# Kernel tuning notes

Measured on AMD Instinct MI355X. Metric: run time of the kernel, lower is better.

Reference implementation:

```python
import jax, jax.numpy as jnp
from jax import lax
import numpy as np

B, T, C, D = 16384, 64, 2, 4  # batch, timesteps(nodes), coords, gat out dim
NEG_SLOPE = 0.2

def setup_inputs() -> dict:
    key = jax.random.key(0)
    ks = jax.random.split(key, 9)
    s = lambda *sh: 0.1
    return {
        "x":      jax.random.normal(ks[0], (B, T, C), jnp.float32),
        "W_gat":  jax.random.normal(ks[1], (D, C), jnp.float32) * 0.5,
        "a_attn": jax.random.normal(ks[2], (1, 2 * D), jnp.float32) * 0.5,
        "conv_w": jax.random.normal(ks[3], (T, T, 3), jnp.float32) * 0.05,
        "conv_b": jax.random.normal(ks[4], (T,), jnp.float32) * 0.05,
        "dec_w1": jax.random.normal(ks[5], (T * 8, T * 2), jnp.float32) * 0.05,
        "dec_b1": jax.random.normal(ks[6], (T * 8,), jnp.float32) * 0.05,
        "dec_w2": jax.random.normal(ks[7], (T * 2, T * 8), jnp.float32) * 0.05,
        "dec_b2": jax.random.normal(ks[8], (T * 2,), jnp.float32) * 0.05,
    }

def reference(x, W_gat, a_attn, conv_w, conv_b, dec_w1, dec_b1, dec_w2, dec_b2):
    b, t, c = x.shape
    # --- GAT layer on fully connected graph (no self loops), batched over B ---
    z = jnp.einsum('btc,dc->btd', x, W_gat)            # [B,T,D]
    a_src, a_dst = a_attn[0, :D], a_attn[0, D:]
    es = z @ a_src                                      # [B,T] contribution of edge source i
    ed = z @ a_dst                                      # [B,T] contribution of edge dest j
    e = jax.nn.leaky_relu(es[:, :, None] + ed[:, None, :], NEG_SLOPE)  # e[b,i,j], edge i->j
    no_self = ~jnp.eye(t, dtype=bool)
    e = jnp.where(no_self[None], e, -jnp.inf)           # graph has no self-loops
    alpha = jax.nn.softmax(e, axis=1)                   # softmax over incoming sources i per dst j
    h = jnp.einsum('bij,bid->bjd', alpha, z)            # [B,T,D] aggregated node features
    # --- conv1d: channels = timesteps, length = D, kernel 3 -> length D-2 ---
    out_conv = lax.conv_general_dilated(h, conv_w, (1,), 'VALID',
                                        dimension_numbers=('NCH', 'OIH', 'NCH'))
    out_conv = out_conv + conv_b[None, :, None]         # [B,T,D-2] == [B,T,2]
    # --- MLP decoder on flattened conv output ---
    flat = out_conv.reshape(b, t * 2)
    hdec = jax.nn.relu(flat @ dec_w1.T + dec_b1)
    dec = hdec @ dec_w2.T + dec_b2
    encoder_out = out_conv[:, None]                     # stacked unsqueeze(0): [B,1,T,2]
    decoded = dec.reshape(b, t, c)                      # [B,T,2]
    return encoder_out, decoded
```

## Files before the change

kernel.cpp:

```cpp
#include <hip/hip_runtime.h>


typedef __attribute__((ext_vector_type(8))) short bf16x8;
typedef __attribute__((ext_vector_type(4))) float f32x4;
typedef _Float16 h2 __attribute__((ext_vector_type(2)));

__device__ __forceinline__ unsigned short f2bf(float f) {
    unsigned int u = __builtin_bit_cast(unsigned int, f);
    return (unsigned short)((u + 0x7FFFu + ((u >> 16) & 1u)) >> 16);
}
__device__ __forceinline__ unsigned int pack2bf(float a, float b) {
    return (unsigned int)f2bf(a) | ((unsigned int)f2bf(b) << 16);
}

#define SWZ(row) (((row) & 7) << 3)

__global__ void k0_prep(const float* __restrict__ w1, const float* __restrict__ w2,
                        const float* __restrict__ cw, const float* __restrict__ cb,
                        unsigned short* __restrict__ w1c, unsigned short* __restrict__ w2c,
                        unsigned short* __restrict__ wcvc, float* __restrict__ biasf) {
    const int i = blockIdx.x * 256 + threadIdx.x;
    const int rem = i & 511, ln = rem >> 3, e = rem & 7;
    const int r = ln & 15, g = ln >> 4;
    {
        const int frag = i >> 9, nb = frag >> 2, kb = frag & 3;
        w1c[i] = f2bf(w1[(nb * 16 + r) * 128 + kb * 32 + g * 8 + e]);
    }
    {
        const int frag = i >> 9, mb = frag >> 4, np = frag & 15;
        w2c[i] = f2bf(w2[(mb * 16 + r) * 512 + np * 32 + g * 8 + e]);
    }
    if (i < 32768) {
        const int frag = i >> 9, fb = frag >> 3, kc = frag & 7;
        const int f = fb * 16 + r, kd = kc * 32 + g * 8 + e;
        const int o = f >> 1, s = f & 1, node = kd >> 2, d = kd & 3;
        const int k = d - s;
        const float v = (k >= 0 && k < 3) ? cw[o * 192 + node * 3 + k] : 0.f;
        wcvc[i] = f2bf(v);
    }
    if (i < 128) biasf[i] = cb[i >> 1];
}

__global__ __launch_bounds__(256, 4) void k_fused(
    const float* __restrict__ x,
    const float* __restrict__ W_gat,
    const float* __restrict__ a_attn,
    const unsigned short* __restrict__ w1c,
    const unsigned short* __restrict__ w2c,
    const unsigned short* __restrict__ wcvc,
    const float* __restrict__ biasf,
    const float* __restrict__ b1,
    const float* __restrict__ b2,
    float* __restrict__ enc_out,
    float* __restrict__ dec_out)
{
    __shared__ __align__(16) unsigned char smem[28672];
    unsigned short* h_lds    = (unsigned short*)smem;
    unsigned short* flat_lds = (unsigned short*)(smem + 8192);
    unsigned short* scr16    = (unsigned short*)(smem + 12288);
    unsigned short* hdec_lds = (unsigned short*)(smem + 12288);

    const int tid = threadIdx.x, lane = tid & 63, wv = tid >> 6;
    const int r = lane & 15, g = lane >> 4;
    const int base = blockIdx.x * 16;
    const int l8 = lane * 8;

    {
        const float Wg00 = W_gat[0], Wg01 = W_gat[1], Wg10 = W_gat[2], Wg11 = W_gat[3];
        const float Wg20 = W_gat[4], Wg21 = W_gat[5], Wg30 = W_gat[6], Wg31 = W_gat[7];
        const float as0 = a_attn[0], as1 = a_attn[1], as2 = a_attn[2], as3 = a_attn[3];
        const float ad0 = a_attn[4], ad1 = a_attn[5], ad2 = a_attn[6], ad3 = a_attn[7];
        const float cs0 = as0 * Wg00 + as1 * Wg10 + as2 * Wg20 + as3 * Wg30;
        const float cs1 = as0 * Wg01 + as1 * Wg11 + as2 * Wg21 + as3 * Wg31;
        const float cd0 = ad0 * Wg00 + ad1 * Wg10 + ad2 * Wg20 + ad3 * Wg30;
        const float cd1 = ad0 * Wg01 + ad1 * Wg11 + ad2 * Wg21 + ad3 * Wg31;
        const float L2E = 1.4426950408889634f;
        const float SL = 0.2f;

        h2 uvh[4], UVh[4], xyh[4];
        float xf0[4], xf1[4];

        #pragma unroll
        for (int t = 0; t < 4; ++t) {
            const float2 xv = ((const float2*)x)[(size_t)(base + wv * 4 + t) * 64 + lane];
            const float es = xv.x * cs0 + xv.y * cs1;
            const float ed = xv.x * cd0 + xv.y * cd1;
            float M = es;
            #pragma unroll
            for (int m = 32; m; m >>= 1) M = fmaxf(M, __shfl_xor(M, m));
            const float um = (es - M) * L2E;
            const _Float16 uh = (_Float16)__builtin_amdgcn_exp2f(um);
            const _Float16 vh = (_Float16)__builtin_amdgcn_exp2f(SL * um);
            const float tt = M + ed;
            const float mj = fmaxf(tt, SL * tt);
            const _Float16 Uh = (_Float16)__builtin_amdgcn_exp2f((ed + M - mj) * L2E);
            const _Float16 Vh = (_Float16)__builtin_amdgcn_exp2f((SL * (ed + M) - mj) * L2E);
            const _Float16 x0h = (_Float16)xv.x, x1h = (_Float16)xv.y;

            unsigned short* rowp = scr16 + (wv * 4 + t) * 256;
            rowp[lane]       = __builtin_bit_cast(unsigned short, uh);
            rowp[64 + lane]  = __builtin_bit_cast(unsigned short, vh);
            rowp[128 + lane] = __builtin_bit_cast(unsigned short, x0h);
            rowp[192 + lane] = __builtin_bit_cast(unsigned short, x1h);

            uvh[t] = (h2){uh, vh};
            UVh[t] = (h2){Uh, Vh};
            xyh[t] = (h2){x0h, x1h};
            xf0[t] = (float)x0h; xf1[t] = (float)x1h;
        }

        const h2 one2 = {(_Float16)1.0f, (_Float16)1.0f};

        #pragma unroll
        for (int t = 0; t < 4; ++t) {
            const uint4* up = (const uint4*)(scr16 + (wv * 4 + t) * 256);
            const h2 UU = (h2){UVh[t].x, UVh[t].x};
            const h2 VV = (h2){UVh[t].y, UVh[t].y};
            float S = 0.f, A0 = 0.f, A1 = 0.f;
            #pragma unroll 4
            for (int k = 0; k < 8; ++k) {
                const uint4 uq  = up[k];
                const uint4 vq  = up[8 + k];
                const uint4 x0q = up[16 + k];
                const uint4 x1q = up[24 + k];
                const unsigned* ua  = (const unsigned*)&uq;
                const unsigned* va  = (const unsigned*)&vq;
                const unsigned* x0a = (const unsigned*)&x0q;
                const unsigned* x1a = (const unsigned*)&x1q;
                #pragma unroll
                for (int p = 0; p < 4; ++p) {
                    const h2 u2  = __builtin_bit_cast(h2, ua[p]);
                    const h2 v2  = __builtin_bit_cast(h2, va[p]);
                    const h2 P2  = __builtin_elementwise_max(u2 * UU, v2 * VV);
#if __has_builtin(__builtin_amdgcn_fdot2)
                    S  = __builtin_amdgcn_fdot2(P2, one2, S, false);
                    A0 = __builtin_amdgcn_fdot2(P2, __builtin_bit_cast(h2, x0a[p]), A0, false);
                    A1 = __builtin_amdgcn_fdot2(P2, __builtin_bit_cast(h2, x1a[p]), A1, false);
#else
                    const h2 xa = __builtin_bit_cast(h2, x0a[p]);
                    const h2 xb = __builtin_bit_cast(h2, x1a[p]);
                    S  += (float)P2.x + (float)P2.y;
                    A0 += (float)P2.x * (float)xa.x + (float)P2.y * (float)xa.y;
                    A1 += (float)P2.x * (float)xb.x + (float)P2.y * (float)xb.y;
#endif
                }
            }
            const h2 pm = uvh[t] * UVh[t];
            const _Float16 pSh = (pm.x > pm.y) ? pm.x : pm.y;
            const float pS = (float)pSh;
            S -= pS;
            A0 -= pS * xf0[t];
            A1 -= pS * xf1[t];
            const float rs = 1.0f / S;
            const float h0 = (Wg00 * A0 + Wg01 * A1) * rs;
            const float h1 = (Wg10 * A0 + Wg11 * A1) * rs;
            const float h2v = (Wg20 * A0 + Wg21 * A1) * rs;
            const float h3 = (Wg30 * A0 + Wg31 * A1) * rs;
            const int lr = wv * 4 + t;
            const int hidx = (lr * 256 + lane * 4) ^ SWZ(lr);
            *(uint2*)(&h_lds[hidx]) = make_uint2(pack2bf(h0, h1), pack2bf(h2v, h3));
        }
    }
    __syncthreads();

    f32x4 accc[2];
    accc[0] = (f32x4){0.f, 0.f, 0.f, 0.f};
    accc[1] = (f32x4){0.f, 0.f, 0.f, 0.f};
    #pragma unroll
    for (int kc = 0; kc < 8; ++kc) {
        const bf16x8 hf  = *(const bf16x8*)(&h_lds[(r * 256 + kc * 32 + g * 8) ^ SWZ(r)]);
        const bf16x8 wfa = *(const bf16x8*)(wcvc + ((wv * 8 + kc) << 9) + l8);
        const bf16x8 wfb = *(const bf16x8*)(wcvc + (((wv + 4) * 8 + kc) << 9) + l8);
        accc[0] = __builtin_amdgcn_mfma_f32_16x16x32_bf16(wfa, hf, accc[0], 0, 0, 0);
        accc[1] = __builtin_amdgcn_mfma_f32_16x16x32_bf16(wfb, hf, accc[1], 0, 0, 0);
    }
    #pragma unroll
    for (int q = 0; q < 2; ++q) {
        const int f0 = (wv + q * 4) * 16 + g * 4;
        const float4 bs = *(const float4*)(biasf + f0);
        const float v0 = accc[q][0] + bs.x, v1 = accc[q][1] + bs.y;
        const float v2 = accc[q][2] + bs.z, v3 = accc[q][3] + bs.w;
        *(float4*)(enc_out + (size_t)(base + r) * 128 + f0) = make_float4(v0, v1, v2, v3);
        const int fidx = (r * 128 + f0) ^ SWZ(r);
        *(uint2*)(&flat_lds[fidx]) = make_uint2(pack2bf(v0, v1), pack2bf(v2, v3));
    }
    __syncthreads();

    bf16x8 ff1[4];
    #pragma unroll
    for (int kb = 0; kb < 4; ++kb)
        ff1[kb] = *(const bf16x8*)(&flat_lds[(r * 128 + kb * 32 + g * 8) ^ SWZ(r)]);
    #pragma unroll
    for (int t = 0; t < 8; ++t) {
        const int nb = wv * 8 + t;
        f32x4 a1 = (f32x4){0.f, 0.f, 0.f, 0.f};
        #pragma unroll
        for (int kb = 0; kb < 4; ++kb) {
            const bf16x8 wf = *(const bf16x8*)(w1c + (((nb << 2) + kb) << 9) + l8);
            a1 = __builtin_amdgcn_mfma_f32_16x16x32_bf16(wf, ff1[kb], a1, 0, 0, 0);
        }
        const int n0 = nb * 16 + g * 4;
        const float4 bs = *(const float4*)(b1 + n0);
        const float v0 = fmaxf(a1[0] + bs.x, 0.f);
        const float v1 = fmaxf(a1[1] + bs.y, 0.f);
        const float v2 = fmaxf(a1[2] + bs.z, 0.f);
        const float v3 = fmaxf(a1[3] + bs.w, 0.f);
        const int hdidx = (r * 512 + n0) ^ SWZ(r);
        *(uint2*)(&hdec_lds[hdidx]) = make_uint2(pack2bf(v0, v1), pack2bf(v2, v3));
    }
    __syncthreads();

    f32x4 acc2[2];
    acc2[0] = (f32x4){0.f, 0.f, 0.f, 0.f};
    acc2[1] = (f32x4){0.f, 0.f, 0.f, 0.f};
    #pragma unroll
    for (int np = 0; np < 16; ++np) {
        const bf16x8 hfd = *(const bf16x8*)(&hdec_lds[(r * 512 + np * 32 + g * 8) ^ SWZ(r)]);
        const bf16x8 wfa = *(const bf16x8*)(w2c + (((wv * 16) + np) << 9) + l8);
        const bf16x8 wfb = *(const bf16x8*)(w2c + ((((wv + 4) * 16) + np) << 9) + l8);
        acc2[0] = __builtin_amdgcn_mfma_f32_16x16x32_bf16(wfa, hfd, acc2[0], 0, 0, 0);
        acc2[1] = __builtin_amdgcn_mfma_f32_16x16x32_bf16(wfb, hfd, acc2[1], 0, 0, 0);
    }
    #pragma unroll
    for (int q = 0; q < 2; ++q) {
        const int m0 = (wv + q * 4) * 16 + g * 4;
        const float4 bs = *(const float4*)(b2 + m0);
        *(float4*)(dec_out + (size_t)(base + r) * 128 + m0) =
            make_float4(acc2[q][0] + bs.x, acc2[q][1] + bs.y,
                        acc2[q][2] + bs.z, acc2[q][3] + bs.w);
    }
}

extern "C" void kernel_launch(void* const* d_in, const int* in_sizes, int n_in,
                              void* d_out, int out_size, void* d_ws, size_t ws_size,
                              hipStream_t stream) {
    const float* x      = (const float*)d_in[0];
    const float* W_gat  = (const float*)d_in[1];
    const float* a_attn = (const float*)d_in[2];
    const float* conv_w = (const float*)d_in[3];
    const float* conv_b = (const float*)d_in[4];
    const float* dec_w1 = (const float*)d_in[5];
    const float* dec_b1 = (const float*)d_in[6];
    const float* dec_w2 = (const float*)d_in[7];
    const float* dec_b2 = (const float*)d_in[8];
    float* out = (float*)d_out;

    const int B = in_sizes[0] / 128;
    unsigned short* w1c  = (unsigned short*)d_ws;
    unsigned short* w2c  = w1c + 128 * 512;
    unsigned short* wcvc = w2c + 128 * 512;
    float* biasf = (float*)(wcvc + 64 * 512);

    k0_prep<<<256, 256, 0, stream>>>(dec_w1, dec_w2, conv_w, conv_b, w1c, w2c, wcvc, biasf);

    k_fused<<<B / 16, 256, 0, stream>>>(x, W_gat, a_attn, w1c, w2c, wcvc, biasf,
                                        dec_b1, dec_b2, out, out + (size_t)B * 128);
}
```

Measured before the change: 31.01 us.

## Process 32 batch rows per block to reuse weight fragments across two MFMA tiles

Each block now handles 32 batch elements instead of 16, so every weight fragment loaded from global memory (conv, dec_w1, dec_w2) feeds two MFMA tiles. The GAT phase is merged into a single per-row loop that prefetches the next x row while computing the current one. Shared memory doubles and launch bounds drop to 2 blocks per CU, which cuts weight-load traffic but halves the block count and may reduce occupancy and latency hiding.

```diff
diff --git a/kernel.cpp b/kernel.cpp
--- a/kernel.cpp
+++ b/kernel.cpp
@@ -41,7 +41,7 @@
     if (i < 128) biasf[i] = cb[i >> 1];
 }
 
-__global__ __launch_bounds__(256, 4) void k_fused(
+__global__ __launch_bounds__(256, 2) void k_fused(
     const float* __restrict__ x,
     const float* __restrict__ W_gat,
     const float* __restrict__ a_attn,
@@ -54,15 +54,15 @@
     float* __restrict__ enc_out,
     float* __restrict__ dec_out)
 {
-    __shared__ __align__(16) unsigned char smem[28672];
+    __shared__ __align__(16) unsigned char smem[57344];
     unsigned short* h_lds    = (unsigned short*)smem;
-    unsigned short* flat_lds = (unsigned short*)(smem + 8192);
-    unsigned short* scr16    = (unsigned short*)(smem + 12288);
-    unsigned short* hdec_lds = (unsigned short*)(smem + 12288);
+    unsigned short* flat_lds = (unsigned short*)(smem + 16384);
+    unsigned short* scr16    = (unsigned short*)(smem + 24576);
+    unsigned short* hdec_lds = (unsigned short*)(smem + 24576);
 
     const int tid = threadIdx.x, lane = tid & 63, wv = tid >> 6;
     const int r = lane & 15, g = lane >> 4;
-    const int base = blockIdx.x * 16;
+    const int base = blockIdx.x * 32;
     const int l8 = lane * 8;
 
     {
@@ -76,13 +76,15 @@
         const float cd1 = ad0 * Wg01 + ad1 * Wg11 + ad2 * Wg21 + ad3 * Wg31;
         const float L2E = 1.4426950408889634f;
         const float SL = 0.2f;
-
-        h2 uvh[4], UVh[4], xyh[4];
-        float xf0[4], xf1[4];
-
-        #pragma unroll
-        for (int t = 0; t < 4; ++t) {
-            const float2 xv = ((const float2*)x)[(size_t)(base + wv * 4 + t) * 64 + lane];
+        const h2 one2 = {(_Float16)1.0f, (_Float16)1.0f};
+
+        float2 xv = ((const float2*)x)[(size_t)(base + wv * 8) * 64 + lane];
+        #pragma unroll
+        for (int t = 0; t < 8; ++t) {
+            float2 xv_n;
+            if (t < 7) xv_n = ((const float2*)x)[(size_t)(base + wv * 8 + t + 1) * 64 + lane];
+            const int lr = wv * 8 + t;
+
             const float es = xv.x * cs0 + xv.y * cs1;
             const float ed = xv.x * cd0 + xv.y * cd1;
             float M = es;
@@ -97,25 +99,15 @@
             const _Float16 Vh = (_Float16)__builtin_amdgcn_exp2f((SL * (ed + M) - mj) * L2E);
             const _Float16 x0h = (_Float16)xv.x, x1h = (_Float16)xv.y;
 
-            unsigned short* rowp = scr16 + (wv * 4 + t) * 256;
+            unsigned short* rowp = scr16 + lr * 256;
             rowp[lane]       = __builtin_bit_cast(unsigned short, uh);
             rowp[64 + lane]  = __builtin_bit_cast(unsigned short, vh);
             rowp[128 + lane] = __builtin_bit_cast(unsigned short, x0h);
             rowp[192 + lane] = __builtin_bit_cast(unsigned short, x1h);
 
-            uvh[t] = (h2){uh, vh};
-            UVh[t] = (h2){Uh, Vh};
-            xyh[t] = (h2){x0h, x1h};
-            xf0[t] = (float)x0h; xf1[t] = (float)x1h;
-        }
-
-        const h2 one2 = {(_Float16)1.0f, (_Float16)1.0f};
-
-        #pragma unroll
-        for (int t = 0; t < 4; ++t) {
-            const uint4* up = (const uint4*)(scr16 + (wv * 4 + t) * 256);
-            const h2 UU = (h2){UVh[t].x, UVh[t].x};
-            const h2 VV = (h2){UVh[t].y, UVh[t].y};
+            const h2 UU = (h2){Uh, Uh};
+            const h2 VV = (h2){Vh, Vh};
+            const uint4* up = (const uint4*)rowp;
             float S = 0.f, A0 = 0.f, A1 = 0.f;
             #pragma unroll 4
             for (int k = 0; k < 8; ++k) {
@@ -129,9 +121,9 @@
                 const unsigned* x1a = (const unsigned*)&x1q;
                 #pragma unroll
                 for (int p = 0; p < 4; ++p) {
-                    const h2 u2  = __builtin_bit_cast(h2, ua[p]);
-                    const h2 v2  = __builtin_bit_cast(h2, va[p]);
-                    const h2 P2  = __builtin_elementwise_max(u2 * UU, v2 * VV);
+                    const h2 u2 = __builtin_bit_cast(h2, ua[p]);
+                    const h2 v2 = __builtin_bit_cast(h2, va[p]);
+                    const h2 P2 = __builtin_elementwise_max(u2 * UU, v2 * VV);
 #if __has_builtin(__builtin_amdgcn_fdot2)
                     S  = __builtin_amdgcn_fdot2(P2, one2, S, false);
                     A0 = __builtin_amdgcn_fdot2(P2, __builtin_bit_cast(h2, x0a[p]), A0, false);
@@ -145,89 +137,115 @@
 #endif
                 }
             }
-            const h2 pm = uvh[t] * UVh[t];
+            const h2 pm = (h2){uh, vh} * (h2){Uh, Vh};
             const _Float16 pSh = (pm.x > pm.y) ? pm.x : pm.y;
             const float pS = (float)pSh;
             S -= pS;
-            A0 -= pS * xf0[t];
-            A1 -= pS * xf1[t];
+            A0 -= pS * (float)x0h;
+            A1 -= pS * (float)x1h;
             const float rs = 1.0f / S;
             const float h0 = (Wg00 * A0 + Wg01 * A1) * rs;
             const float h1 = (Wg10 * A0 + Wg11 * A1) * rs;
             const float h2v = (Wg20 * A0 + Wg21 * A1) * rs;
             const float h3 = (Wg30 * A0 + Wg31 * A1) * rs;
-            const int lr = wv * 4 + t;
             const int hidx = (lr * 256 + lane * 4) ^ SWZ(lr);
             *(uint2*)(&h_lds[hidx]) = make_uint2(pack2bf(h0, h1), pack2bf(h2v, h3));
+            xv = xv_n;
         }
     }
     __syncthreads();
 
-    f32x4 accc[2];
-    accc[0] = (f32x4){0.f, 0.f, 0.f, 0.f};
-    accc[1] = (f32x4){0.f, 0.f, 0.f, 0.f};
+    f32x4 accc[2][2];
+    #pragma unroll
+    for (int q = 0; q < 2; ++q)
+        #pragma unroll
+        for (int tl = 0; tl < 2; ++tl) accc[q][tl] = (f32x4){0.f, 0.f, 0.f, 0.f};
     #pragma unroll
     for (int kc = 0; kc < 8; ++kc) {
-        const bf16x8 hf  = *(const bf16x8*)(&h_lds[(r * 256 + kc * 32 + g * 8) ^ SWZ(r)]);
         const bf16x8 wfa = *(const bf16x8*)(wcvc + ((wv * 8 + kc) << 9) + l8);
         const bf16x8 wfb = *(const bf16x8*)(wcvc + (((wv + 4) * 8 + kc) << 9) + l8);
-        accc[0] = __builtin_amdgcn_mfma_f32_16x16x32_bf16(wfa, hf, accc[0], 0, 0, 0);
-        accc[1] = __builtin_amdgcn_mfma_f32_16x16x32_bf16(wfb, hf, accc[1], 0, 0, 0);
+        #pragma unroll
+        for (int tl = 0; tl < 2; ++tl) {
+            const int row = tl * 16 + r;
+            const bf16x8 hf = *(const bf16x8*)(&h_lds[(row * 256 + kc * 32 + g * 8) ^ SWZ(r)]);
+            accc[0][tl] = __builtin_amdgcn_mfma_f32_16x16x32_bf16(wfa, hf, accc[0][tl], 0, 0, 0);
+            accc[1][tl] = __builtin_amdgcn_mfma_f32_16x16x32_bf16(wfb, hf, accc[1][tl], 0, 0, 0);
+        }
     }
     #pragma unroll
     for (int q = 0; q < 2; ++q) {
         const int f0 = (wv + q * 4) * 16 + g * 4;
         const float4 bs = *(const float4*)(biasf + f0);
-        const float v0 = accc[q][0] + bs.x, v1 = accc[q][1] + bs.y;
-        const float v2 = accc[q][2] + bs.z, v3 = accc[q][3] + bs.w;
-        *(float4*)(enc_out + (size_t)(base + r) * 128 + f0) = make_float4(v0, v1, v2, v3);
-        const int fidx = (r * 128 + f0) ^ SWZ(r);
-        *(uint2*)(&flat_lds[fidx]) = make_uint2(pack2bf(v0, v1), pack2bf(v2, v3));
+        #pragma unroll
+        for (int tl = 0; tl < 2; ++tl) {
+            const int row = tl * 16 + r;
+            const float v0 = accc[q][tl][0] + bs.x, v1 = accc[q][tl][1] + bs.y;
+            const float v2 = accc[q][tl][2] + bs.z, v3 = accc[q][tl][3] + bs.w;
+            *(float4*)(enc_out + (size_t)(base + row) * 128 + f0) = make_float4(v0, v1, v2, v3);
+            const int fidx = (row * 128 + f0) ^ SWZ(r);
+            *(uint2*)(&flat_lds[fidx]) = make_uint2(pack2bf(v0, v1), pack2bf(v2, v3));
+        }
     }
     __syncthreads();
 
-    bf16x8 ff1[4];
-    #pragma unroll
-    for (int kb = 0; kb < 4; ++kb)
-        ff1[kb] = *(const bf16x8*)(&flat_lds[(r * 128 + kb * 32 + g * 8) ^ SWZ(r)]);
+    bf16x8 ff1[2][4];
+    #pragma unroll
+    for (int tl = 0; tl < 2; ++tl)
+        #pragma unroll
+        for (int kb = 0; kb < 4; ++kb)
+            ff1[tl][kb] = *(const bf16x8*)(&flat_lds[((tl * 16 + r) * 128 + kb * 32 + g * 8) ^ SWZ(r)]);
     #pragma unroll
     for (int t = 0; t < 8; ++t) {
         const int nb = wv * 8 + t;
-        f32x4 a1 = (f32x4){0.f, 0.f, 0.f, 0.f};
+        f32x4 a1[2];
+        a1[0] = (f32x4){0.f, 0.f, 0.f, 0.f};
+        a1[1] = (f32x4){0.f, 0.f, 0.f, 0.f};
         #pragma unroll
         for (int kb = 0; kb < 4; ++kb) {
             const bf16x8 wf = *(const bf16x8*)(w1c + (((nb << 2) + kb) << 9) + l8);
-            a1 = __builtin_amdgcn_mfma_f32_16x16x32_bf16(wf, ff1[kb], a1, 0, 0, 0);
+            a1[0] = __builtin_amdgcn_mfma_f32_16x16x32_bf16(wf, ff1[0][kb], a1[0], 0, 0, 0);
+            a1[1] = __builtin_amdgcn_mfma_f32_16x16x32_bf16(wf, ff1[1][kb], a1[1], 0, 0, 0);
         }
         const int n0 = nb * 16 + g * 4;
         const float4 bs = *(const float4*)(b1 + n0);
-        const float v0 = fmaxf(a1[0] + bs.x, 0.f);
-        const float v1 = fmaxf(a1[1] + bs.y, 0.f);
-        const float v2 = fmaxf(a1[2] + bs.z, 0.f);
-        const float v3 = fmaxf(a1[3] + bs.w, 0.f);
-        const int hdidx = (r * 512 + n0) ^ SWZ(r);
-        *(uint2*)(&hdec_lds[hdidx]) = make_uint2(pack2bf(v0, v1), pack2bf(v2, v3));
+        #pragma unroll
+        for (int tl = 0; tl < 2; ++tl) {
+            const float v0 = fmaxf(a1[tl][0] + bs.x, 0.f);
+            const float v1 = fmaxf(a1[tl][1] + bs.y, 0.f);
+            const float v2 = fmaxf(a1[tl][2] + bs.z, 0.f);
+            const float v3 = fmaxf(a1[tl][3] + bs.w, 0.f);
+            const int hdidx = ((tl * 16 + r) * 512 + n0) ^ SWZ(r);
+            *(uint2*)(&hdec_lds[hdidx]) = make_uint2(pack2bf(v0, v1), pack2bf(v2, v3));
+        }
     }
     __syncthreads();
 
-    f32x4 acc2[2];
-    acc2[0] = (f32x4){0.f, 0.f, 0.f, 0.f};
-    acc2[1] = (f32x4){0.f, 0.f, 0.f, 0.f};
+    f32x4 acc2[2][2];
+    #pragma unroll
+    for (int q = 0; q < 2; ++q)
+        #pragma unroll
+        for (int tl = 0; tl < 2; ++tl) acc2[q][tl] = (f32x4){0.f, 0.f, 0.f, 0.f};
     #pragma unroll
     for (int np = 0; np < 16; ++np) {
-        const bf16x8 hfd = *(const bf16x8*)(&hdec_lds[(r * 512 + np * 32 + g * 8) ^ SWZ(r)]);
         const bf16x8 wfa = *(const bf16x8*)(w2c + (((wv * 16) + np) << 9) + l8);
         const bf16x8 wfb = *(const bf16x8*)(w2c + ((((wv + 4) * 16) + np) << 9) + l8);
-        acc2[0] = __builtin_amdgcn_mfma_f32_16x16x32_bf16(wfa, hfd, acc2[0], 0, 0, 0);
-        acc2[1] = __builtin_amdgcn_mfma_f32_16x16x32_bf16(wfb, hfd, acc2[1], 0, 0, 0);
+        #pragma unroll
+        for (int tl = 0; tl < 2; ++tl) {
+            const bf16x8 hfd = *(const bf16x8*)(&hdec_lds[((tl * 16 + r) * 512 + np * 32 + g * 8) ^ SWZ(r)]);
+            acc2[0][tl] = __builtin_amdgcn_mfma_f32_16x16x32_bf16(wfa, hfd, acc2[0][tl], 0, 0, 0);
+            acc2[1][tl] = __builtin_amdgcn_mfma_f32_16x16x32_bf16(wfb, hfd, acc2[1][tl], 0, 0, 0);
+        }
     }
     #pragma unroll
     for (int q = 0; q < 2; ++q) {
         const int m0 = (wv + q * 4) * 16 + g * 4;
         const float4 bs = *(const float4*)(b2 + m0);
-        *(float4*)(dec_out + (size_t)(base + r) * 128 + m0) =
-            make_float4(acc2[q][0] + bs.x, acc2[q][1] + bs.y,
-                        acc2[q][2] + bs.z, acc2[q][3] + bs.w);
+        #pragma unroll
+        for (int tl = 0; tl < 2; ++tl) {
+            *(float4*)(dec_out + (size_t)(base + tl * 16 + r) * 128 + m0) =
+                make_float4(acc2[q][tl][0] + bs.x, acc2[q][tl][1] + bs.y,
+                            acc2[q][tl][2] + bs.z, acc2[q][tl][3] + bs.w);
+        }
     }
 }
 
@@ -253,6 +271,6 @@
 
     k0_prep<<<256, 256, 0, stream>>>(dec_w1, dec_w2, conv_w, conv_b, w1c, w2c, wcvc, biasf);
 
-    k_fused<<<B / 16, 256, 0, stream>>>(x, W_gat, a_attn, w1c, w2c, wcvc, biasf,
+    k_fused<<<B / 32, 256, 0, stream>>>(x, W_gat, a_attn, w1c, w2c, wcvc, biasf,
                                         dec_b1, dec_b2, out, out + (size_t)B * 128);
 }
```

Measured after the change: 32.16 us. 3.7% more time.

## Split fused kernel work across eight waves per block instead of four

Applied to the files above, without the earlier changes.

Launches 512 threads per block so each wave handles two batch rows in the GAT stage and half as many output tiles in the conv and decoder MFMA stages. The per-wave MFMA chains are split into two independent accumulators over K halves to shorten dependency chains, and the next x row is prefetched before the current one is processed. The aim is more waves in flight and less serial work per wave to hide latency. In exchange, the larger block with launch bounds (512,3) changes the register budget and occupancy, and the block-wide syncs now cover more waves.

```diff
diff --git a/kernel.cpp b/kernel.cpp
--- a/kernel.cpp
+++ b/kernel.cpp
@@ -41,7 +41,7 @@
     if (i < 128) biasf[i] = cb[i >> 1];
 }
 
-__global__ __launch_bounds__(256, 4) void k_fused(
+__global__ __launch_bounds__(512, 3) void k_fused(
     const float* __restrict__ x,
     const float* __restrict__ W_gat,
     const float* __restrict__ a_attn,
@@ -76,13 +76,15 @@
         const float cd1 = ad0 * Wg01 + ad1 * Wg11 + ad2 * Wg21 + ad3 * Wg31;
         const float L2E = 1.4426950408889634f;
         const float SL = 0.2f;
-
-        h2 uvh[4], UVh[4], xyh[4];
-        float xf0[4], xf1[4];
-
+        const h2 one2 = {(_Float16)1.0f, (_Float16)1.0f};
+
+        float2 xv = ((const float2*)x)[(size_t)(base + wv * 2) * 64 + lane];
         #pragma unroll
-        for (int t = 0; t < 4; ++t) {
-            const float2 xv = ((const float2*)x)[(size_t)(base + wv * 4 + t) * 64 + lane];
+        for (int t = 0; t < 2; ++t) {
+            float2 xv_n;
+            if (t == 0) xv_n = ((const float2*)x)[(size_t)(base + wv * 2 + 1) * 64 + lane];
+            const int lr = wv * 2 + t;
+
             const float es = xv.x * cs0 + xv.y * cs1;
             const float ed = xv.x * cd0 + xv.y * cd1;
             float M = es;
@@ -97,25 +99,15 @@
             const _Float16 Vh = (_Float16)__builtin_amdgcn_exp2f((SL * (ed + M) - mj) * L2E);
             const _Float16 x0h = (_Float16)xv.x, x1h = (_Float16)xv.y;
 
-            unsigned short* rowp = scr16 + (wv * 4 + t) * 256;
+            unsigned short* rowp = scr16 + lr * 256;
             rowp[lane]       = __builtin_bit_cast(unsigned short, uh);
             rowp[64 + lane]  = __builtin_bit_cast(unsigned short, vh);
             rowp[128 + lane] = __builtin_bit_cast(unsigned short, x0h);
             rowp[192 + lane] = __builtin_bit_cast(unsigned short, x1h);
 
-            uvh[t] = (h2){uh, vh};
-            UVh[t] = (h2){Uh, Vh};
-            xyh[t] = (h2){x0h, x1h};
-            xf0[t] = (float)x0h; xf1[t] = (float)x1h;
-        }
-
-        const h2 one2 = {(_Float16)1.0f, (_Float16)1.0f};
-
-        #pragma unroll
-        for (int t = 0; t < 4; ++t) {
-            const uint4* up = (const uint4*)(scr16 + (wv * 4 + t) * 256);
-            const h2 UU = (h2){UVh[t].x, UVh[t].x};
-            const h2 VV = (h2){UVh[t].y, UVh[t].y};
+            const h2 UU = (h2){Uh, Uh};
+            const h2 VV = (h2){Vh, Vh};
+            const uint4* up = (const uint4*)rowp;
             float S = 0.f, A0 = 0.f, A1 = 0.f;
             #pragma unroll 4
             for (int k = 0; k < 8; ++k) {
@@ -129,9 +121,9 @@
                 const unsigned* x1a = (const unsigned*)&x1q;
                 #pragma unroll
                 for (int p = 0; p < 4; ++p) {
-                    const h2 u2  = __builtin_bit_cast(h2, ua[p]);
-                    const h2 v2  = __builtin_bit_cast(h2, va[p]);
-                    const h2 P2  = __builtin_elementwise_max(u2 * UU, v2 * VV);
+                    const h2 u2 = __builtin_bit_cast(h2, ua[p]);
+                    const h2 v2 = __builtin_bit_cast(h2, va[p]);
+                    const h2 P2 = __builtin_elementwise_max(u2 * UU, v2 * VV);
 #if __has_builtin(__builtin_amdgcn_fdot2)
                     S  = __builtin_amdgcn_fdot2(P2, one2, S, false);
                     A0 = __builtin_amdgcn_fdot2(P2, __builtin_bit_cast(h2, x0a[p]), A0, false);
@@ -145,41 +137,41 @@
 #endif
                 }
             }
-            const h2 pm = uvh[t] * UVh[t];
+            const h2 pm = (h2){uh, vh} * (h2){Uh, Vh};
             const _Float16 pSh = (pm.x > pm.y) ? pm.x : pm.y;
             const float pS = (float)pSh;
             S -= pS;
-            A0 -= pS * xf0[t];
-            A1 -= pS * xf1[t];
+            A0 -= pS * (float)x0h;
+            A1 -= pS * (float)x1h;
             const float rs = 1.0f / S;
             const float h0 = (Wg00 * A0 + Wg01 * A1) * rs;
             const float h1 = (Wg10 * A0 + Wg11 * A1) * rs;
             const float h2v = (Wg20 * A0 + Wg21 * A1) * rs;
             const float h3 = (Wg30 * A0 + Wg31 * A1) * rs;
-            const int lr = wv * 4 + t;
             const int hidx = (lr * 256 + lane * 4) ^ SWZ(lr);
             *(uint2*)(&h_lds[hidx]) = make_uint2(pack2bf(h0, h1), pack2bf(h2v, h3));
+            xv = xv_n;
         }
     }
     __syncthreads();
 
-    f32x4 accc[2];
-    accc[0] = (f32x4){0.f, 0.f, 0.f, 0.f};
-    accc[1] = (f32x4){0.f, 0.f, 0.f, 0.f};
-    #pragma unroll
-    for (int kc = 0; kc < 8; ++kc) {
-        const bf16x8 hf  = *(const bf16x8*)(&h_lds[(r * 256 + kc * 32 + g * 8) ^ SWZ(r)]);
-        const bf16x8 wfa = *(const bf16x8*)(wcvc + ((wv * 8 + kc) << 9) + l8);
-        const bf16x8 wfb = *(const bf16x8*)(wcvc + (((wv + 4) * 8 + kc) << 9) + l8);
-        accc[0] = __builtin_amdgcn_mfma_f32_16x16x32_bf16(wfa, hf, accc[0], 0, 0, 0);
-        accc[1] = __builtin_amdgcn_mfma_f32_16x16x32_bf16(wfb, hf, accc[1], 0, 0, 0);
-    }
-    #pragma unroll
-    for (int q = 0; q < 2; ++q) {
-        const int f0 = (wv + q * 4) * 16 + g * 4;
+    f32x4 ca = (f32x4){0.f, 0.f, 0.f, 0.f};
+    f32x4 cb2 = (f32x4){0.f, 0.f, 0.f, 0.f};
+    #pragma unroll
+    for (int kc = 0; kc < 4; ++kc) {
+        const bf16x8 hf0 = *(const bf16x8*)(&h_lds[(r * 256 + kc * 32 + g * 8) ^ SWZ(r)]);
+        const bf16x8 hf1 = *(const bf16x8*)(&h_lds[(r * 256 + (kc + 4) * 32 + g * 8) ^ SWZ(r)]);
+        const bf16x8 wf0 = *(const bf16x8*)(wcvc + ((wv * 8 + kc) << 9) + l8);
+        const bf16x8 wf1 = *(const bf16x8*)(wcvc + ((wv * 8 + kc + 4) << 9) + l8);
+        ca  = __builtin_amdgcn_mfma_f32_16x16x32_bf16(wf0, hf0, ca, 0, 0, 0);
+        cb2 = __builtin_amdgcn_mfma_f32_16x16x32_bf16(wf1, hf1, cb2, 0, 0, 0);
+    }
+    {
+        const f32x4 cc = ca + cb2;
+        const int f0 = wv * 16 + g * 4;
         const float4 bs = *(const float4*)(biasf + f0);
-        const float v0 = accc[q][0] + bs.x, v1 = accc[q][1] + bs.y;
-        const float v2 = accc[q][2] + bs.z, v3 = accc[q][3] + bs.w;
+        const float v0 = cc[0] + bs.x, v1 = cc[1] + bs.y;
+        const float v2 = cc[2] + bs.z, v3 = cc[3] + bs.w;
         *(float4*)(enc_out + (size_t)(base + r) * 128 + f0) = make_float4(v0, v1, v2, v3);
         const int fidx = (r * 128 + f0) ^ SWZ(r);
         *(uint2*)(&flat_lds[fidx]) = make_uint2(pack2bf(v0, v1), pack2bf(v2, v3));
@@ -191,8 +183,8 @@
     for (int kb = 0; kb < 4; ++kb)
         ff1[kb] = *(const bf16x8*)(&flat_lds[(r * 128 + kb * 32 + g * 8) ^ SWZ(r)]);
     #pragma unroll
-    for (int t = 0; t < 8; ++t) {
-        const int nb = wv * 8 + t;
+    for (int t = 0; t < 4; ++t) {
+        const int nb = wv * 4 + t;
         f32x4 a1 = (f32x4){0.f, 0.f, 0.f, 0.f};
         #pragma unroll
         for (int kb = 0; kb < 4; ++kb) {
@@ -210,24 +202,23 @@
     }
     __syncthreads();
 
-    f32x4 acc2[2];
-    acc2[0] = (f32x4){0.f, 0.f, 0.f, 0.f};
-    acc2[1] = (f32x4){0.f, 0.f, 0.f, 0.f};
-    #pragma unroll
-    for (int np = 0; np < 16; ++np) {
-        const bf16x8 hfd = *(const bf16x8*)(&hdec_lds[(r * 512 + np * 32 + g * 8) ^ SWZ(r)]);
-        const bf16x8 wfa = *(const bf16x8*)(w2c + (((wv * 16) + np) << 9) + l8);
-        const bf16x8 wfb = *(const bf16x8*)(w2c + ((((wv + 4) * 16) + np) << 9) + l8);
-        acc2[0] = __builtin_amdgcn_mfma_f32_16x16x32_bf16(wfa, hfd, acc2[0], 0, 0, 0);
-        acc2[1] = __builtin_amdgcn_mfma_f32_16x16x32_bf16(wfb, hfd, acc2[1], 0, 0, 0);
-    }
-    #pragma unroll
-    for (int q = 0; q < 2; ++q) {
-        const int m0 = (wv + q * 4) * 16 + g * 4;
+    f32x4 d2a = (f32x4){0.f, 0.f, 0.f, 0.f};
+    f32x4 d2b = (f32x4){0.f, 0.f, 0.f, 0.f};
+    #pragma unroll
+    for (int np = 0; np < 8; ++np) {
+        const bf16x8 h0 = *(const bf16x8*)(&hdec_lds[(r * 512 + np * 32 + g * 8) ^ SWZ(r)]);
+        const bf16x8 h1 = *(const bf16x8*)(&hdec_lds[(r * 512 + (np + 8) * 32 + g * 8) ^ SWZ(r)]);
+        const bf16x8 w0 = *(const bf16x8*)(w2c + (((wv * 16) + np) << 9) + l8);
+        const bf16x8 w1 = *(const bf16x8*)(w2c + (((wv * 16) + np + 8) << 9) + l8);
+        d2a = __builtin_amdgcn_mfma_f32_16x16x32_bf16(w0, h0, d2a, 0, 0, 0);
+        d2b = __builtin_amdgcn_mfma_f32_16x16x32_bf16(w1, h1, d2b, 0, 0, 0);
+    }
+    {
+        const f32x4 dd = d2a + d2b;
+        const int m0 = wv * 16 + g * 4;
         const float4 bs = *(const float4*)(b2 + m0);
         *(float4*)(dec_out + (size_t)(base + r) * 128 + m0) =
-            make_float4(acc2[q][0] + bs.x, acc2[q][1] + bs.y,
-                        acc2[q][2] + bs.z, acc2[q][3] + bs.w);
+            make_float4(dd[0] + bs.x, dd[1] + bs.y, dd[2] + bs.z, dd[3] + bs.w);
     }
 }
 
@@ -253,6 +244,6 @@
 
     k0_prep<<<256, 256, 0, stream>>>(dec_w1, dec_w2, conv_w, conv_b, w1c, w2c, wcvc, biasf);
 
-    k_fused<<<B / 16, 256, 0, stream>>>(x, W_gat, a_attn, w1c, w2c, wcvc, biasf,
+    k_fused<<<B / 16, 512, 0, stream>>>(x, W_gat, a_attn, w1c, w2c, wcvc, biasf,
                                         dec_b1, dec_b2, out, out + (size_t)B * 128);
 }
```

New measurement: 32.53 us. 1.05x slower.

## Split fused kernel into attention and conv/decoder kernels via global staging

Applied to the files above, without the earlier changes.

The fused kernel is split in two. The first computes the GAT attention and writes bf16 h values in MFMA fragment order into the decoded output region as scratch. The second reads h directly from global memory for the conv MFMAs and then runs the decoder. The aim is lower register and LDS pressure per kernel and a software-prefetched x load. The cost is an extra launch plus a global round trip for h, and the scratch buffer relies on being overwritten in place, since the second kernel reads h from the same region it writes decoded results into.

```diff
diff --git a/kernel.cpp b/kernel.cpp
--- a/kernel.cpp
+++ b/kernel.cpp
@@ -41,10 +41,110 @@
     if (i < 128) biasf[i] = cb[i >> 1];
 }
 
-__global__ __launch_bounds__(256, 4) void k_fused(
+__global__ __launch_bounds__(256, 4) void k_attn(
     const float* __restrict__ x,
     const float* __restrict__ W_gat,
     const float* __restrict__ a_attn,
+    unsigned int* __restrict__ h_frag)
+{
+    __shared__ unsigned short scr16[16 * 256];
+
+    const int tid = threadIdx.x, lane = tid & 63, wv = tid >> 6;
+    const int base = blockIdx.x * 16;
+
+    const float Wg00 = W_gat[0], Wg01 = W_gat[1], Wg10 = W_gat[2], Wg11 = W_gat[3];
+    const float Wg20 = W_gat[4], Wg21 = W_gat[5], Wg30 = W_gat[6], Wg31 = W_gat[7];
+    const float as0 = a_attn[0], as1 = a_attn[1], as2 = a_attn[2], as3 = a_attn[3];
+    const float ad0 = a_attn[4], ad1 = a_attn[5], ad2 = a_attn[6], ad3 = a_attn[7];
+    const float cs0 = as0 * Wg00 + as1 * Wg10 + as2 * Wg20 + as3 * Wg30;
+    const float cs1 = as0 * Wg01 + as1 * Wg11 + as2 * Wg21 + as3 * Wg31;
+    const float cd0 = ad0 * Wg00 + ad1 * Wg10 + ad2 * Wg20 + ad3 * Wg30;
+    const float cd1 = ad0 * Wg01 + ad1 * Wg11 + ad2 * Wg21 + ad3 * Wg31;
+    const float L2E = 1.4426950408889634f;
+    const float SL = 0.2f;
+    const h2 one2 = {(_Float16)1.0f, (_Float16)1.0f};
+
+    const int j = lane;
+    unsigned int* outp = h_frag + (size_t)blockIdx.x * 2048
+                       + (j >> 3) * 256 + ((j >> 1) & 3) * 64 + (j & 1) * 2;
+
+    float2 xv = ((const float2*)x)[(size_t)(base + wv * 4) * 64 + lane];
+    #pragma unroll
+    for (int t = 0; t < 4; ++t) {
+        float2 xv_n;
+        if (t < 3) xv_n = ((const float2*)x)[(size_t)(base + wv * 4 + t + 1) * 64 + lane];
+        const int lr = wv * 4 + t;
+
+        const float es = xv.x * cs0 + xv.y * cs1;
+        const float ed = xv.x * cd0 + xv.y * cd1;
+        float M = es;
+        #pragma unroll
+        for (int m = 32; m; m >>= 1) M = fmaxf(M, __shfl_xor(M, m));
+        const float um = (es - M) * L2E;
+        const _Float16 uh = (_Float16)__builtin_amdgcn_exp2f(um);
+        const _Float16 vh = (_Float16)__builtin_amdgcn_exp2f(SL * um);
+        const float tt = M + ed;
+        const float mj = fmaxf(tt, SL * tt);
+        const _Float16 Uh = (_Float16)__builtin_amdgcn_exp2f((ed + M - mj) * L2E);
+        const _Float16 Vh = (_Float16)__builtin_amdgcn_exp2f((SL * (ed + M) - mj) * L2E);
+        const _Float16 x0h = (_Float16)xv.x, x1h = (_Float16)xv.y;
+
+        unsigned short* rowp = scr16 + lr * 256;
+        rowp[lane]       = __builtin_bit_cast(unsigned short, uh);
+        rowp[64 + lane]  = __builtin_bit_cast(unsigned short, vh);
+        rowp[128 + lane] = __builtin_bit_cast(unsigned short, x0h);
+        rowp[192 + lane] = __builtin_bit_cast(unsigned short, x1h);
+
+        const h2 UU = (h2){Uh, Uh};
+        const h2 VV = (h2){Vh, Vh};
+        const uint4* up = (const uint4*)rowp;
+        float S = 0.f, A0 = 0.f, A1 = 0.f;
+        #pragma unroll 4
+        for (int k = 0; k < 8; ++k) {
+            const uint4 uq  = up[k];
+            const uint4 vq  = up[8 + k];
+            const uint4 x0q = up[16 + k];
+            const uint4 x1q = up[24 + k];
+            const unsigned* ua  = (const unsigned*)&uq;
+            const unsigned* va  = (const unsigned*)&vq;
+            const unsigned* x0a = (const unsigned*)&x0q;
+            const unsigned* x1a = (const unsigned*)&x1q;
+            #pragma unroll
+            for (int p = 0; p < 4; ++p) {
+                const h2 u2 = __builtin_bit_cast(h2, ua[p]);
+                const h2 v2 = __builtin_bit_cast(h2, va[p]);
+                const h2 P2 = __builtin_elementwise_max(u2 * UU, v2 * VV);
+#if __has_builtin(__builtin_amdgcn_fdot2)
+                S  = __builtin_amdgcn_fdot2(P2, one2, S, false);
+                A0 = __builtin_amdgcn_fdot2(P2, __builtin_bit_cast(h2, x0a[p]), A0, false);
+                A1 = __builtin_amdgcn_fdot2(P2, __builtin_bit_cast(h2, x1a[p]), A1, false);
+#else
+                const h2 xa = __builtin_bit_cast(h2, x0a[p]);
+                const h2 xb = __builtin_bit_cast(h2, x1a[p]);
+                S  += (float)P2.x + (float)P2.y;
+                A0 += (float)P2.x * (float)xa.x + (float)P2.y * (float)xa.y;
+                A1 += (float)P2.x * (float)xb.x + (float)P2.y * (float)xb.y;
+#endif
+            }
+        }
+        const h2 pm = (h2){uh, vh} * (h2){Uh, Vh};
+        const _Float16 pSh = (pm.x > pm.y) ? pm.x : pm.y;
+        const float pS = (float)pSh;
+        S -= pS;
+        A0 -= pS * (float)x0h;
+        A1 -= pS * (float)x1h;
+        const float rs = 1.0f / S;
+        const float h0 = (Wg00 * A0 + Wg01 * A1) * rs;
+        const float h1 = (Wg10 * A0 + Wg11 * A1) * rs;
+        const float h2v = (Wg20 * A0 + Wg21 * A1) * rs;
+        const float h3 = (Wg30 * A0 + Wg31 * A1) * rs;
+        *(uint2*)(outp + lr * 4) = make_uint2(pack2bf(h0, h1), pack2bf(h2v, h3));
+        xv = xv_n;
+    }
+}
+
+__global__ __launch_bounds__(256, 4) void k_convdec(
+    const unsigned short* h_bf,
     const unsigned short* __restrict__ w1c,
     const unsigned short* __restrict__ w2c,
     const unsigned short* __restrict__ wcvc,
@@ -52,123 +152,23 @@
     const float* __restrict__ b1,
     const float* __restrict__ b2,
     float* __restrict__ enc_out,
-    float* __restrict__ dec_out)
+    float* dec_out)
 {
-    __shared__ __align__(16) unsigned char smem[28672];
-    unsigned short* h_lds    = (unsigned short*)smem;
-    unsigned short* flat_lds = (unsigned short*)(smem + 8192);
-    unsigned short* scr16    = (unsigned short*)(smem + 12288);
-    unsigned short* hdec_lds = (unsigned short*)(smem + 12288);
+    __shared__ unsigned short flat_lds[16 * 128];
+    __shared__ unsigned short hdec_lds[16 * 512];
 
     const int tid = threadIdx.x, lane = tid & 63, wv = tid >> 6;
     const int r = lane & 15, g = lane >> 4;
     const int base = blockIdx.x * 16;
     const int l8 = lane * 8;
-
-    {
-        const float Wg00 = W_gat[0], Wg01 = W_gat[1], Wg10 = W_gat[2], Wg11 = W_gat[3];
-        const float Wg20 = W_gat[4], Wg21 = W_gat[5], Wg30 = W_gat[6], Wg31 = W_gat[7];
-        const float as0 = a_attn[0], as1 = a_attn[1], as2 = a_attn[2], as3 = a_attn[3];
-        const float ad0 = a_attn[4], ad1 = a_attn[5], ad2 = a_attn[6], ad3 = a_attn[7];
-        const float cs0 = as0 * Wg00 + as1 * Wg10 + as2 * Wg20 + as3 * Wg30;
-        const float cs1 = as0 * Wg01 + as1 * Wg11 + as2 * Wg21 + as3 * Wg31;
-        const float cd0 = ad0 * Wg00 + ad1 * Wg10 + ad2 * Wg20 + ad3 * Wg30;
-        const float cd1 = ad0 * Wg01 + ad1 * Wg11 + ad2 * Wg21 + ad3 * Wg31;
-        const float L2E = 1.4426950408889634f;
-        const float SL = 0.2f;
-
-        h2 uvh[4], UVh[4], xyh[4];
-        float xf0[4], xf1[4];
-
-        #pragma unroll
-        for (int t = 0; t < 4; ++t) {
-            const float2 xv = ((const float2*)x)[(size_t)(base + wv * 4 + t) * 64 + lane];
-            const float es = xv.x * cs0 + xv.y * cs1;
-            const float ed = xv.x * cd0 + xv.y * cd1;
-            float M = es;
-            #pragma unroll
-            for (int m = 32; m; m >>= 1) M = fmaxf(M, __shfl_xor(M, m));
-            const float um = (es - M) * L2E;
-            const _Float16 uh = (_Float16)__builtin_amdgcn_exp2f(um);
-            const _Float16 vh = (_Float16)__builtin_amdgcn_exp2f(SL * um);
-            const float tt = M + ed;
-            const float mj = fmaxf(tt, SL * tt);
-            const _Float16 Uh = (_Float16)__builtin_amdgcn_exp2f((ed + M - mj) * L2E);
-            const _Float16 Vh = (_Float16)__builtin_amdgcn_exp2f((SL * (ed + M) - mj) * L2E);
-            const _Float16 x0h = (_Float16)xv.x, x1h = (_Float16)xv.y;
-
-            unsigned short* rowp = scr16 + (wv * 4 + t) * 256;
-            rowp[lane]       = __builtin_bit_cast(unsigned short, uh);
-            rowp[64 + lane]  = __builtin_bit_cast(unsigned short, vh);
-            rowp[128 + lane] = __builtin_bit_cast(unsigned short, x0h);
-            rowp[192 + lane] = __builtin_bit_cast(unsigned short, x1h);
-
-            uvh[t] = (h2){uh, vh};
-            UVh[t] = (h2){Uh, Vh};
-            xyh[t] = (h2){x0h, x1h};
-            xf0[t] = (float)x0h; xf1[t] = (float)x1h;
-        }
-
-        const h2 one2 = {(_Float16)1.0f, (_Float16)1.0f};
-
-        #pragma unroll
-        for (int t = 0; t < 4; ++t) {
-            const uint4* up = (const uint4*)(scr16 + (wv * 4 + t) * 256);
-            const h2 UU = (h2){UVh[t].x, UVh[t].x};
-            const h2 VV = (h2){UVh[t].y, UVh[t].y};
-            float S = 0.f, A0 = 0.f, A1 = 0.f;
-            #pragma unroll 4
-            for (int k = 0; k < 8; ++k) {
-                const uint4 uq  = up[k];
-                const uint4 vq  = up[8 + k];
-                const uint4 x0q = up[16 + k];
-                const uint4 x1q = up[24 + k];
-                const unsigned* ua  = (const unsigned*)&uq;
-                const unsigned* va  = (const unsigned*)&vq;
-                const unsigned* x0a = (const unsigned*)&x0q;
-                const unsigned* x1a = (const unsigned*)&x1q;
-                #pragma unroll
-                for (int p = 0; p < 4; ++p) {
-                    const h2 u2  = __builtin_bit_cast(h2, ua[p]);
-                    const h2 v2  = __builtin_bit_cast(h2, va[p]);
-                    const h2 P2  = __builtin_elementwise_max(u2 * UU, v2 * VV);
-#if __has_builtin(__builtin_amdgcn_fdot2)
-                    S  = __builtin_amdgcn_fdot2(P2, one2, S, false);
-                    A0 = __builtin_amdgcn_fdot2(P2, __builtin_bit_cast(h2, x0a[p]), A0, false);
-                    A1 = __builtin_amdgcn_fdot2(P2, __builtin_bit_cast(h2, x1a[p]), A1, false);
-#else
-                    const h2 xa = __builtin_bit_cast(h2, x0a[p]);
-                    const h2 xb = __builtin_bit_cast(h2, x1a[p]);
-                    S  += (float)P2.x + (float)P2.y;
-                    A0 += (float)P2.x * (float)xa.x + (float)P2.y * (float)xa.y;
-                    A1 += (float)P2.x * (float)xb.x + (float)P2.y * (float)xb.y;
-#endif
-                }
-            }
-            const h2 pm = uvh[t] * UVh[t];
-            const _Float16 pSh = (pm.x > pm.y) ? pm.x : pm.y;
-            const float pS = (float)pSh;
-            S -= pS;
-            A0 -= pS * xf0[t];
-            A1 -= pS * xf1[t];
-            const float rs = 1.0f / S;
-            const float h0 = (Wg00 * A0 + Wg01 * A1) * rs;
-            const float h1 = (Wg10 * A0 + Wg11 * A1) * rs;
-            const float h2v = (Wg20 * A0 + Wg21 * A1) * rs;
-            const float h3 = (Wg30 * A0 + Wg31 * A1) * rs;
-            const int lr = wv * 4 + t;
-            const int hidx = (lr * 256 + lane * 4) ^ SWZ(lr);
-            *(uint2*)(&h_lds[hidx]) = make_uint2(pack2bf(h0, h1), pack2bf(h2v, h3));
-        }
-    }
-    __syncthreads();
+    const unsigned short* htile = h_bf + (size_t)blockIdx.x * 4096;
 
     f32x4 accc[2];
     accc[0] = (f32x4){0.f, 0.f, 0.f, 0.f};
     accc[1] = (f32x4){0.f, 0.f, 0.f, 0.f};
     #pragma unroll
     for (int kc = 0; kc < 8; ++kc) {
-        const bf16x8 hf  = *(const bf16x8*)(&h_lds[(r * 256 + kc * 32 + g * 8) ^ SWZ(r)]);
+        const bf16x8 hf  = *(const bf16x8*)(htile + kc * 512 + l8);
         const bf16x8 wfa = *(const bf16x8*)(wcvc + ((wv * 8 + kc) << 9) + l8);
         const bf16x8 wfb = *(const bf16x8*)(wcvc + (((wv + 4) * 8 + kc) << 9) + l8);
         accc[0] = __builtin_amdgcn_mfma_f32_16x16x32_bf16(wfa, hf, accc[0], 0, 0, 0);
@@ -251,8 +251,12 @@
     unsigned short* wcvc = w2c + 128 * 512;
     float* biasf = (float*)(wcvc + 64 * 512);
 
+    unsigned short* h_bf = (unsigned short*)(out + (size_t)B * 128);
+
     k0_prep<<<256, 256, 0, stream>>>(dec_w1, dec_w2, conv_w, conv_b, w1c, w2c, wcvc, biasf);
 
-    k_fused<<<B / 16, 256, 0, stream>>>(x, W_gat, a_attn, w1c, w2c, wcvc, biasf,
-                                        dec_b1, dec_b2, out, out + (size_t)B * 128);
-}
+    k_attn<<<B / 16, 256, 0, stream>>>(x, W_gat, a_attn, (unsigned int*)h_bf);
+
+    k_convdec<<<B / 16, 256, 0, stream>>>(h_bf, w1c, w2c, wcvc, biasf, dec_b1, dec_b2,
+                                          out, out + (size_t)B * 128);
+}
```

Measured after the change: 39.92 us. 1.29x slower.
